# Optimization experiments

Measured on AMD Instinct MI355X. Metric: run time of the kernel, lower is better.

The kernel has to match this reference:

```python
import jax, jax.numpy as jnp
import numpy as np

MARGIN = 1.0
CURVATURE = 1.0
BOUNDARY_FACTOR = 2.0
MARGIN_THRESHOLD = 0.1
EPS = 1e-7


def setup_inputs() -> dict:
    key = jax.random.key(0)
    k1, k2 = jax.random.split(key)
    B, D = 4096, 128
    # scale so norms stay inside the unit Poincare ball (~0.57 on average)
    embeddings = jax.random.normal(k1, (B, D), dtype=jnp.float32) * 0.05
    labels = jax.random.randint(k2, (B,), 0, 64, dtype=jnp.int64)
    return {"embeddings": embeddings, "labels": labels}


def _poincare_distance_matrix(x, c):
    # d(x,y) = (1/sqrt(c)) * arccosh(1 + 2c||x-y||^2 / ((1-c||x||^2)(1-c||y||^2)))
    sq = jnp.sum(x * x, axis=-1)                       # [B]
    diff_sq = jnp.maximum(sq[:, None] + sq[None, :] - 2.0 * (x @ x.T), 0.0)
    denom = jnp.maximum((1.0 - c * sq[:, None]) * (1.0 - c * sq[None, :]), EPS)
    arg = 1.0 + 2.0 * c * diff_sq / denom
    return jnp.arccosh(jnp.maximum(arg, 1.0)) / jnp.sqrt(c)


def reference(embeddings, labels):
    B = embeddings.shape[0]
    distances = _poincare_distance_matrix(embeddings, CURVATURE)   # [B,B]

    same = labels[:, None] == labels[None, :]
    eye = jnp.eye(B, dtype=bool)
    positive_mask = same & ~eye
    negative_mask = ~same

    has_pos = jnp.any(positive_mask, axis=1)
    has_neg = jnp.any(negative_mask, axis=1)
    valid_anchor = has_pos & has_neg                               # [B]

    neg_inf = jnp.asarray(-jnp.inf, distances.dtype)
    hardest_pos = jnp.max(jnp.where(positive_mask, distances, neg_inf), axis=1)
    hardest_pos = jnp.where(has_pos, hardest_pos, 0.0)

    # adaptive margin (torch uses .item() -> detached from autograd)
    anchor_norm = jax.lax.stop_gradient(jnp.linalg.norm(embeddings, axis=-1))
    margin = jnp.maximum(MARGIN * (1.0 + BOUNDARY_FACTOR * anchor_norm),
                         MARGIN_THRESHOLD)                          # [B]

    pair_mask = valid_anchor[:, None] & negative_mask               # [B,B]
    raw = hardest_pos[:, None] - distances + margin[:, None]
    losses = jnp.maximum(raw, 0.0)

    total_triplets = jnp.sum(pair_mask)
    num_active = jnp.sum((raw > 0.0) & pair_mask)
    denom = jnp.maximum(total_triplets, 1).astype(losses.dtype)
    loss = jnp.sum(jnp.where(pair_mask, losses, 0.0)) / denom       # 'mean'

    active_ratio = num_active.astype(jnp.float32) / jnp.maximum(
        total_triplets.astype(jnp.float32), 1.0)
    pos_count = jnp.sum(positive_mask)
    mean_distance = jnp.where(
        pos_count > 0,
        jnp.sum(jnp.where(positive_mask, distances, 0.0))
        / jnp.maximum(pos_count, 1).astype(distances.dtype),
        0.0)

    return (loss, num_active, total_triplets, active_ratio, mean_distance)
```

## Files before the change

kernel.cpp:

```cpp
#include <hip/hip_runtime.h>
#include <hip/hip_bf16.h>
#include <math.h>

static constexpr int D        = 128;
static constexpr int NL       = 64;
static constexpr int NT       = 64;
static constexpr int NT2      = 128;
static constexpr int LIDX_CAP = 512;

typedef __attribute__((ext_vector_type(8))) short  bf16x8;
typedef __attribute__((ext_vector_type(4))) float  f32x4;

__device__ __forceinline__ float wave_reduce_sum(float v) {
  #pragma unroll
  for (int o = 32; o; o >>= 1) v += __shfl_xor(v, o, 64);
  return v;
}

__device__ __forceinline__ float fast_acosh(float x) {
  float s = __builtin_amdgcn_sqrtf(fmaf(x, x, -1.0f));
  return __logf(x + s);
}

__device__ __forceinline__ unsigned short f2b(float x) {
  unsigned int u = __float_as_uint(x);
  unsigned int lsb = (u >> 16) & 1u;
  u += 0x7fffu + lsb;
  return (unsigned short)(u >> 16);
}
__device__ __forceinline__ float b2f(unsigned short u) {
  return __uint_as_float(((unsigned int)u) << 16);
}

__global__ __launch_bounds__(256) void kA(
    const float* __restrict__ emb, const int* __restrict__ lab,
    unsigned short* __restrict__ bfe, float* __restrict__ sq,
    float* __restrict__ vv, float* __restrict__ hpm,
    int* __restrict__ LC, float* __restrict__ plsum, int B) {
  const int t = threadIdx.x;
  const int bid = blockIdx.x;

  if (bid >= NL) {
    int w = t >> 6, lane = t & 63;
    int i = (bid - NL) * 4 + w;
    float2 v = reinterpret_cast<const float2*>(emb + (size_t)i * D)[lane];
    ushort2 bv = { f2b(v.x), f2b(v.y) };
    *reinterpret_cast<ushort2*>(&bfe[(size_t)i * D + 2 * lane]) = bv;
    float s = wave_reduce_sum(v.x * v.x + v.y * v.y);
    if (lane == 0) {
      sq[i] = s;
      vv[i] = 1.41421356237f / fmaxf(1.0f - s, 1e-6f);
    }
    return;
  }

  __shared__ unsigned short Al[NT][D + 8];
  __shared__ unsigned short Bl[NT][D + 8];
  __shared__ float rs[NT], rv[NT];
  __shared__ float cs[NT], cv[NT];
  __shared__ int   ridx[NT], cidx[NT];
  __shared__ int   lidx[LIDX_CAP];
  __shared__ int   parr[256];
  __shared__ float red[8];

  const int l = bid;
  const int wid = t >> 6, lane = t & 63;
  const int lr = lane & 15, lg = lane >> 4;

  int mc = 0;
  for (int i = t; i < B; i += 256) mc += (lab[i] == l) ? 1 : 0;
  parr[t] = mc;
  __syncthreads();
  for (int off = 1; off < 256; off <<= 1) {
    int v = (t >= off) ? parr[t - off] : 0;
    __syncthreads();
    parr[t] += v;
    __syncthreads();
  }
  const int c = parr[255];
  {
    int myoff = parr[t] - mc;
    for (int i = t; i < B; i += 256) {
      if (lab[i] == l) {
        if (myoff < LIDX_CAP) lidx[myoff] = i;
        ++myoff;
      }
    }
  }
  if (t == 0) { LC[l] = c; if (c == 0) plsum[l] = 0.0f; }
  if (c == 0) return;
  __syncthreads();

  const int  cc_    = min(c, LIDX_CAP);
  const bool validc = (c >= 2) && (c < B);
  float lsum = 0.0f;

  for (int i0 = 0; i0 < cc_; i0 += NT) {
    int ci = min(NT, cc_ - i0);
    __syncthreads();
    #pragma unroll
    for (int p = 0; p < 4; ++p) {
      int idx = t + p * 256;
      int r = idx >> 4, c16 = idx & 15;
      const float* src = emb + (size_t)lidx[i0 + min(r, ci - 1)] * D + c16 * 8;
      float4 a = *reinterpret_cast<const float4*>(src);
      float4 b = *reinterpret_cast<const float4*>(src + 4);
      ushort4 ua = { f2b(a.x), f2b(a.y), f2b(a.z), f2b(a.w) };
      ushort4 ub = { f2b(b.x), f2b(b.y), f2b(b.z), f2b(b.w) };
      *reinterpret_cast<ushort4*>(&Al[r][c16 * 8]) = ua;
      *reinterpret_cast<ushort4*>(&Al[r][c16 * 8 + 4]) = ub;
    }
    __syncthreads();
    {
      int r = t >> 2, q = t & 3;
      float s = 0.0f;
      #pragma unroll
      for (int i = 0; i < 4; ++i) {
        bf16x8 v8 = *reinterpret_cast<const bf16x8*>(&Al[r][q * 32 + i * 8]);
        #pragma unroll
        for (int j = 0; j < 8; ++j) {
          float x = b2f((unsigned short)v8[j]);
          s = fmaf(x, x, s);
        }
      }
      s += __shfl_xor(s, 1, 64);
      s += __shfl_xor(s, 2, 64);
      if (q == 0) {
        rs[r] = s;
        rv[r] = 1.41421356237f / fmaxf(1.0f - s, 1e-6f);
        ridx[r] = lidx[i0 + min(r, ci - 1)];
      }
    }

    float rmax[4] = {0.0f, 0.0f, 0.0f, 0.0f};

    for (int j0 = 0; j0 < cc_; j0 += NT) {
      int cj = min(NT, cc_ - j0);
      __syncthreads();
      #pragma unroll
      for (int p = 0; p < 4; ++p) {
        int idx = t + p * 256;
        int r = idx >> 4, c16 = idx & 15;
        const float* src = emb + (size_t)lidx[j0 + min(r, cj - 1)] * D + c16 * 8;
        float4 a = *reinterpret_cast<const float4*>(src);
        float4 b = *reinterpret_cast<const float4*>(src + 4);
        ushort4 ua = { f2b(a.x), f2b(a.y), f2b(a.z), f2b(a.w) };
        ushort4 ub = { f2b(b.x), f2b(b.y), f2b(b.z), f2b(b.w) };
        *reinterpret_cast<ushort4*>(&Bl[r][c16 * 8]) = ua;
        *reinterpret_cast<ushort4*>(&Bl[r][c16 * 8 + 4]) = ub;
      }
      __syncthreads();
      {
        int r = t >> 2, q = t & 3;
        float s = 0.0f;
        #pragma unroll
        for (int i = 0; i < 4; ++i) {
          bf16x8 v8 = *reinterpret_cast<const bf16x8*>(&Bl[r][q * 32 + i * 8]);
          #pragma unroll
          for (int j = 0; j < 8; ++j) {
            float x = b2f((unsigned short)v8[j]);
            s = fmaf(x, x, s);
          }
        }
        s += __shfl_xor(s, 1, 64);
        s += __shfl_xor(s, 2, 64);
        if (q == 0) {
          cs[r] = s;
          cv[r] = 1.41421356237f / fmaxf(1.0f - s, 1e-6f);
          cidx[r] = lidx[j0 + min(r, cj - 1)];
        }
      }
      __syncthreads();

      f32x4 dacc[4];
      #pragma unroll
      for (int n = 0; n < 4; ++n) dacc[n] = (f32x4){0.f, 0.f, 0.f, 0.f};
      #pragma unroll
      for (int kk = 0; kk < 4; ++kk) {
        bf16x8 a = *reinterpret_cast<const bf16x8*>(&Al[wid * 16 + lr][kk * 32 + lg * 8]);
        bf16x8 b[4];
        #pragma unroll
        for (int n = 0; n < 4; ++n)
          b[n] = *reinterpret_cast<const bf16x8*>(&Bl[n * 16 + lr][kk * 32 + lg * 8]);
        #pragma unroll
        for (int n = 0; n < 4; ++n)
          dacc[n] = __builtin_amdgcn_mfma_f32_16x16x32_bf16(a, b[n], dacc[n], 0, 0, 0);
      }

      int r0 = wid * 16 + lg * 4;
      #pragma unroll
      for (int n = 0; n < 4; ++n) {
        int ccn = n * 16 + lr;
        float sc = cs[ccn], vcv = cv[ccn];
        int   gj = cidx[ccn];
        #pragma unroll
        for (int g = 0; g < 4; ++g) {
          int rloc = r0 + g;
          if (rloc < ci && ccn < cj && ridx[rloc] != gj) {
            float diff = fmaxf(fmaf(-2.0f, dacc[n][g], rs[rloc] + sc), 0.0f);
            float arg  = fmaf(diff * rv[rloc], vcv, 1.0f);
            float d    = fast_acosh(arg);
            lsum += d;
            rmax[g] = fmaxf(rmax[g], d);
          }
        }
      }
    }

    int r0 = wid * 16 + lg * 4;
    #pragma unroll
    for (int g = 0; g < 4; ++g) {
      float v = rmax[g];
      v = fmaxf(v, __shfl_xor(v, 1, 64));
      v = fmaxf(v, __shfl_xor(v, 2, 64));
      v = fmaxf(v, __shfl_xor(v, 4, 64));
      v = fmaxf(v, __shfl_xor(v, 8, 64));
      int rloc = r0 + g;
      if (lr == 0 && rloc < ci) {
        float mg = fmaxf(fmaf(2.0f, __builtin_amdgcn_sqrtf(rs[rloc]), 1.0f), 0.1f);
        hpm[ridx[rloc]] = validc ? (v + mg) : -1e30f;
      }
    }
  }

  lsum = wave_reduce_sum(lsum);
  if (lane == 0) red[wid] = lsum;
  __syncthreads();
  if (t == 0) plsum[l] = (red[0] + red[1]) + (red[2] + red[3]);
}

__global__ __launch_bounds__(512) void k3_neg(
    const unsigned short* __restrict__ bfe, const int* __restrict__ lab,
    const float* __restrict__ sq, const float* __restrict__ vv,
    const float* __restrict__ hpm,
    float* __restrict__ part, int B) {
  __shared__ unsigned short Al[NT2][D + 8];
  __shared__ unsigned short Bl[NT2][D + 8];
  __shared__ float rs[NT2], rv[NT2], rh[NT2];
  __shared__ float cs[NT2], cv[NT2], ch[NT2];
  __shared__ int   rl[NT2], cl[NT2];
  __shared__ float red[16];

  const int T2 = B / NT2;
  const int t = threadIdx.x;
  const int wid = t >> 6, lane = t & 63;
  const int wr = wid >> 2, wc = wid & 3;
  const int lr = lane & 15, lg = lane >> 4;
  const int bid = blockIdx.x;

  float disc = (float)((2 * T2 + 1) * (2 * T2 + 1) - 8 * bid);
  int bi = (int)(((float)(2 * T2 + 1) - __builtin_amdgcn_sqrtf(disc)) * 0.5f);
  bi = max(0, min(bi, T2 - 1));
  while (bi * T2 - bi * (bi - 1) / 2 > bid) --bi;
  while ((bi + 1) * T2 - (bi + 1) * bi / 2 <= bid) ++bi;
  int bj = bi + (bid - (bi * T2 - bi * (bi - 1) / 2));
  const float dsec = (bi == bj) ? 0.0f : 1.0f;

  const unsigned short* ab = bfe + (size_t)bi * NT2 * D;
  const unsigned short* bb = bfe + (size_t)bj * NT2 * D;
  #pragma unroll
  for (int p = 0; p < 4; ++p) {
    int idx = t + p * 512;
    int r = idx >> 4, c16 = idx & 15;
    bf16x8 va = reinterpret_cast<const bf16x8*>(ab + (size_t)r * D)[c16];
    bf16x8 vb = reinterpret_cast<const bf16x8*>(bb + (size_t)r * D)[c16];
    *reinterpret_cast<bf16x8*>(&Al[r][c16 * 8]) = va;
    *reinterpret_cast<bf16x8*>(&Bl[r][c16 * 8]) = vb;
  }
  if (t < NT2) {
    int g = bi * NT2 + t;
    rs[t] = sq[g]; rv[t] = vv[g]; rh[t] = hpm[g]; rl[t] = lab[g];
  } else if (t < 2 * NT2) {
    int r = t - NT2, g = bj * NT2 + r;
    cs[r] = sq[g]; cv[r] = vv[g]; ch[r] = hpm[g]; cl[r] = lab[g];
  }
  __syncthreads();

  f32x4 dacc[4][2];
  #pragma unroll
  for (int m = 0; m < 4; ++m)
    #pragma unroll
    for (int n = 0; n < 2; ++n) dacc[m][n] = (f32x4){0.f, 0.f, 0.f, 0.f};

  #pragma unroll
  for (int kk = 0; kk < 4; ++kk) {
    bf16x8 a[4], b[2];
    #pragma unroll
    for (int m = 0; m < 4; ++m)
      a[m] = *reinterpret_cast<const bf16x8*>(&Al[wr * 64 + m * 16 + lr][kk * 32 + lg * 8]);
    #pragma unroll
    for (int n = 0; n < 2; ++n)
      b[n] = *reinterpret_cast<const bf16x8*>(&Bl[wc * 32 + n * 16 + lr][kk * 32 + lg * 8]);
    #pragma unroll
    for (int m = 0; m < 4; ++m)
      #pragma unroll
      for (int n = 0; n < 2; ++n)
        dacc[m][n] = __builtin_amdgcn_mfma_f32_16x16x32_bf16(a[m], b[n], dacc[m][n], 0, 0, 0);
  }

  float nsum = 0.0f, nact = 0.0f;
  #pragma unroll
  for (int m = 0; m < 4; ++m) {
    int r0 = wr * 64 + m * 16 + lg * 4;
    f32x4 sr = *reinterpret_cast<const f32x4*>(&rs[r0]);
    f32x4 vr = *reinterpret_cast<const f32x4*>(&rv[r0]);
    f32x4 hr = *reinterpret_cast<const f32x4*>(&rh[r0]);
    int4  lm = *reinterpret_cast<const int4*>(&rl[r0]);
    int lmv[4] = { lm.x, lm.y, lm.z, lm.w };
    #pragma unroll
    for (int n = 0; n < 2; ++n) {
      int ccn = wc * 32 + n * 16 + lr;
      float sc = cs[ccn], vcv = cv[ccn], hc = ch[ccn];
      int   lc = cl[ccn];
      #pragma unroll
      for (int g = 0; g < 4; ++g) {
        float diff = fmaxf(fmaf(-2.0f, dacc[m][n][g], sr[g] + sc), 0.0f);
        float arg  = fmaf(diff * vr[g], vcv, 1.0f);
        float d    = fast_acosh(arg);
        float r1   = hr[g] - d;
        float r2   = hc    - d;
        float neg  = (lmv[g] != lc) ? 1.0f : 0.0f;
        nsum += neg * (fmaxf(r1, 0.0f) + dsec * fmaxf(r2, 0.0f));
        nact += neg * ((r1 > 0.0f ? 1.0f : 0.0f) + dsec * (r2 > 0.0f ? 1.0f : 0.0f));
      }
    }
  }

  nsum = wave_reduce_sum(nsum);
  nact = wave_reduce_sum(nact);
  if (lane == 0) { red[wid] = nsum; red[8 + wid] = nact; }
  __syncthreads();
  if (t == 0) {
    float S = 0.0f, A = 0.0f;
    #pragma unroll
    for (int w = 0; w < 8; ++w) { S += red[w]; A += red[8 + w]; }
    part[2 * bid]     = S;
    part[2 * bid + 1] = A;
  }
}

__global__ __launch_bounds__(256) void k4_final(
    const float* __restrict__ part, int G,
    const int* __restrict__ LC, const float* __restrict__ plsum,
    float* __restrict__ out, int B) {
  __shared__ float sl[256], sa[256];
  __shared__ float fin[3];
  int t = threadIdx.x;
  float s = 0.0f, a = 0.0f;
  for (int i = t; i < G; i += 256) {
    s += part[2 * i];
    a += part[2 * i + 1];
  }
  sl[t] = s; sa[t] = a;
  __syncthreads();
  for (int o = 128; o; o >>= 1) {
    if (t < o) { sl[t] += sl[t + o]; sa[t] += sa[t + o]; }
    __syncthreads();
  }
  if (t < 64) {
    int   c  = LC[t];
    float cf = (float)c;
    float pc = cf * (cf - 1.0f);
    float tr = ((c >= 2) && (c < B)) ? cf * (float)(B - c) : 0.0f;
    float ps = plsum[t];
    pc = wave_reduce_sum(pc);
    tr = wave_reduce_sum(tr);
    ps = wave_reduce_sum(ps);
    if (t == 0) { fin[0] = pc; fin[1] = tr; fin[2] = ps; }
  }
  __syncthreads();
  if (t == 0) {
    float PC = fin[0], TR = fin[1], PS = fin[2];
    float den = fmaxf(TR, 1.0f);
    out[0] = sl[0] / den;
    out[1] = sa[0];
    out[2] = TR;
    out[3] = sa[0] / den;
    out[4] = (PC > 0.0f) ? PS / fmaxf(PC, 1.0f) : 0.0f;
  }
}

extern "C" void kernel_launch(void* const* d_in, const int* in_sizes, int n_in,
                              void* d_out, int out_size, void* d_ws, size_t ws_size,
                              hipStream_t stream) {
  const float* emb = (const float*)d_in[0];
  const int*   lab = (const int*)d_in[1];
  int B = in_sizes[1];

  int T2 = B / NT2;
  int ntile = T2 * (T2 + 1) / 2;

  unsigned short* bfe = (unsigned short*)d_ws;
  float* sq    = (float*)(bfe + (size_t)B * D);
  float* vv    = sq + B;
  float* hpm   = vv + B;
  int*   LC    = (int*)(hpm + B);
  float* plsum = (float*)(LC + NL);
  float* part  = plsum + NL;

  kA<<<NL + B / 4, 256, 0, stream>>>(emb, lab, bfe, sq, vv, hpm, LC, plsum, B);
  k3_neg<<<ntile, 512, 0, stream>>>(bfe, lab, sq, vv, hpm, part, B);
  k4_final<<<1, 256, 0, stream>>>(part, ntile, LC, plsum, (float*)d_out, B);
}
```

Baseline: 44.19 us.

## Make pairwise tile kernel persistent with register-prefetched next tile

The negative-pair kernel now launches a fixed grid of 512 blocks that stride over the 528 upper-triangular tiles instead of one block per tile. While storing the current tile's bf16 rows and per-row scalars to shared memory, each block issues global loads for its next tile into registers, so load latency can overlap compute. The final reduction now sums only G partials. Since 528 is only slightly more than 512, most blocks process one tile and a few process two, which can lengthen the tail, and the prefetch registers raise register pressure.

```diff
diff --git a/kernel.cpp b/kernel.cpp
--- a/kernel.cpp
+++ b/kernel.cpp
@@ -233,7 +233,7 @@
     const unsigned short* __restrict__ bfe, const int* __restrict__ lab,
     const float* __restrict__ sq, const float* __restrict__ vv,
     const float* __restrict__ hpm,
-    float* __restrict__ part, int B) {
+    float* __restrict__ part, int B, int G) {
   __shared__ unsigned short Al[NT2][D + 8];
   __shared__ unsigned short Bl[NT2][D + 8];
   __shared__ float rs[NT2], rv[NT2], rh[NT2];
@@ -242,88 +242,127 @@
   __shared__ float red[16];
 
   const int T2 = B / NT2;
+  const int ntile = T2 * (T2 + 1) / 2;
   const int t = threadIdx.x;
   const int wid = t >> 6, lane = t & 63;
   const int wr = wid >> 2, wc = wid & 3;
   const int lr = lane & 15, lg = lane >> 4;
   const int bid = blockIdx.x;
 
-  float disc = (float)((2 * T2 + 1) * (2 * T2 + 1) - 8 * bid);
-  int bi = (int)(((float)(2 * T2 + 1) - __builtin_amdgcn_sqrtf(disc)) * 0.5f);
-  bi = max(0, min(bi, T2 - 1));
-  while (bi * T2 - bi * (bi - 1) / 2 > bid) --bi;
-  while ((bi + 1) * T2 - (bi + 1) * bi / 2 <= bid) ++bi;
-  int bj = bi + (bid - (bi * T2 - bi * (bi - 1) / 2));
-  const float dsec = (bi == bj) ? 0.0f : 1.0f;
-
-  const unsigned short* ab = bfe + (size_t)bi * NT2 * D;
-  const unsigned short* bb = bfe + (size_t)bj * NT2 * D;
-  #pragma unroll
-  for (int p = 0; p < 4; ++p) {
-    int idx = t + p * 512;
-    int r = idx >> 4, c16 = idx & 15;
-    bf16x8 va = reinterpret_cast<const bf16x8*>(ab + (size_t)r * D)[c16];
-    bf16x8 vb = reinterpret_cast<const bf16x8*>(bb + (size_t)r * D)[c16];
-    *reinterpret_cast<bf16x8*>(&Al[r][c16 * 8]) = va;
-    *reinterpret_cast<bf16x8*>(&Bl[r][c16 * 8]) = vb;
-  }
-  if (t < NT2) {
-    int g = bi * NT2 + t;
-    rs[t] = sq[g]; rv[t] = vv[g]; rh[t] = hpm[g]; rl[t] = lab[g];
-  } else if (t < 2 * NT2) {
-    int r = t - NT2, g = bj * NT2 + r;
-    cs[r] = sq[g]; cv[r] = vv[g]; ch[r] = hpm[g]; cl[r] = lab[g];
-  }
-  __syncthreads();
-
-  f32x4 dacc[4][2];
-  #pragma unroll
-  for (int m = 0; m < 4; ++m)
-    #pragma unroll
-    for (int n = 0; n < 2; ++n) dacc[m][n] = (f32x4){0.f, 0.f, 0.f, 0.f};
-
-  #pragma unroll
-  for (int kk = 0; kk < 4; ++kk) {
-    bf16x8 a[4], b[2];
+  bf16x8 pre[8];
+  float ps0 = 0, ps1 = 0, ps2 = 0;
+  int   ps3 = 0;
+  float nsum = 0.0f, nact = 0.0f;
+
+  auto decode = [&](int tile, int& bi, int& bj) {
+    float disc = (float)((2 * T2 + 1) * (2 * T2 + 1) - 8 * tile);
+    int b = (int)(((float)(2 * T2 + 1) - __builtin_amdgcn_sqrtf(disc)) * 0.5f);
+    b = max(0, min(b, T2 - 1));
+    while (b * T2 - b * (b - 1) / 2 > tile) --b;
+    while ((b + 1) * T2 - (b + 1) * b / 2 <= tile) ++b;
+    bi = b;
+    bj = b + (tile - (b * T2 - b * (b - 1) / 2));
+  };
+
+  auto load_tile = [&](int bi, int bj) {
+    const unsigned short* ab = bfe + (size_t)bi * NT2 * D;
+    const unsigned short* bb = bfe + (size_t)bj * NT2 * D;
+    #pragma unroll
+    for (int p = 0; p < 4; ++p) {
+      int idx = t + p * 512;
+      int r = idx >> 4, c16 = idx & 15;
+      pre[p]     = reinterpret_cast<const bf16x8*>(ab + (size_t)r * D)[c16];
+      pre[4 + p] = reinterpret_cast<const bf16x8*>(bb + (size_t)r * D)[c16];
+    }
+    if (t < NT2) {
+      int g = bi * NT2 + t;
+      ps0 = sq[g]; ps1 = vv[g]; ps2 = hpm[g]; ps3 = lab[g];
+    } else if (t < 2 * NT2) {
+      int g = bj * NT2 + (t - NT2);
+      ps0 = sq[g]; ps1 = vv[g]; ps2 = hpm[g]; ps3 = lab[g];
+    }
+  };
+
+  int tile = bid;
+  if (tile >= ntile) return;
+  int bi, bj;
+  decode(tile, bi, bj);
+  float next_dsec = (bi == bj) ? 0.0f : 1.0f;
+  load_tile(bi, bj);
+
+  while (tile < ntile) {
+    const float dsec = next_dsec;
+    __syncthreads();
+    #pragma unroll
+    for (int p = 0; p < 4; ++p) {
+      int idx = t + p * 512;
+      int r = idx >> 4, c16 = idx & 15;
+      *reinterpret_cast<bf16x8*>(&Al[r][c16 * 8]) = pre[p];
+      *reinterpret_cast<bf16x8*>(&Bl[r][c16 * 8]) = pre[4 + p];
+    }
+    if (t < NT2) {
+      rs[t] = ps0; rv[t] = ps1; rh[t] = ps2; rl[t] = ps3;
+    } else if (t < 2 * NT2) {
+      int r = t - NT2;
+      cs[r] = ps0; cv[r] = ps1; ch[r] = ps2; cl[r] = ps3;
+    }
+    int tile_next = tile + G;
+    if (tile_next < ntile) {
+      decode(tile_next, bi, bj);
+      next_dsec = (bi == bj) ? 0.0f : 1.0f;
+      load_tile(bi, bj);
+    }
+    __syncthreads();
+
+    f32x4 dacc[4][2];
     #pragma unroll
     for (int m = 0; m < 4; ++m)
-      a[m] = *reinterpret_cast<const bf16x8*>(&Al[wr * 64 + m * 16 + lr][kk * 32 + lg * 8]);
-    #pragma unroll
-    for (int n = 0; n < 2; ++n)
-      b[n] = *reinterpret_cast<const bf16x8*>(&Bl[wc * 32 + n * 16 + lr][kk * 32 + lg * 8]);
-    #pragma unroll
-    for (int m = 0; m < 4; ++m)
+      #pragma unroll
+      for (int n = 0; n < 2; ++n) dacc[m][n] = (f32x4){0.f, 0.f, 0.f, 0.f};
+
+    #pragma unroll
+    for (int kk = 0; kk < 4; ++kk) {
+      bf16x8 a[4], b[2];
+      #pragma unroll
+      for (int m = 0; m < 4; ++m)
+        a[m] = *reinterpret_cast<const bf16x8*>(&Al[wr * 64 + m * 16 + lr][kk * 32 + lg * 8]);
       #pragma unroll
       for (int n = 0; n < 2; ++n)
-        dacc[m][n] = __builtin_amdgcn_mfma_f32_16x16x32_bf16(a[m], b[n], dacc[m][n], 0, 0, 0);
-  }
-
-  float nsum = 0.0f, nact = 0.0f;
-  #pragma unroll
-  for (int m = 0; m < 4; ++m) {
-    int r0 = wr * 64 + m * 16 + lg * 4;
-    f32x4 sr = *reinterpret_cast<const f32x4*>(&rs[r0]);
-    f32x4 vr = *reinterpret_cast<const f32x4*>(&rv[r0]);
-    f32x4 hr = *reinterpret_cast<const f32x4*>(&rh[r0]);
-    int4  lm = *reinterpret_cast<const int4*>(&rl[r0]);
-    int lmv[4] = { lm.x, lm.y, lm.z, lm.w };
-    #pragma unroll
-    for (int n = 0; n < 2; ++n) {
-      int ccn = wc * 32 + n * 16 + lr;
-      float sc = cs[ccn], vcv = cv[ccn], hc = ch[ccn];
-      int   lc = cl[ccn];
-      #pragma unroll
-      for (int g = 0; g < 4; ++g) {
-        float diff = fmaxf(fmaf(-2.0f, dacc[m][n][g], sr[g] + sc), 0.0f);
-        float arg  = fmaf(diff * vr[g], vcv, 1.0f);
-        float d    = fast_acosh(arg);
-        float r1   = hr[g] - d;
-        float r2   = hc    - d;
-        float neg  = (lmv[g] != lc) ? 1.0f : 0.0f;
-        nsum += neg * (fmaxf(r1, 0.0f) + dsec * fmaxf(r2, 0.0f));
-        nact += neg * ((r1 > 0.0f ? 1.0f : 0.0f) + dsec * (r2 > 0.0f ? 1.0f : 0.0f));
-      }
-    }
+        b[n] = *reinterpret_cast<const bf16x8*>(&Bl[wc * 32 + n * 16 + lr][kk * 32 + lg * 8]);
+      #pragma unroll
+      for (int m = 0; m < 4; ++m)
+        #pragma unroll
+        for (int n = 0; n < 2; ++n)
+          dacc[m][n] = __builtin_amdgcn_mfma_f32_16x16x32_bf16(a[m], b[n], dacc[m][n], 0, 0, 0);
+    }
+
+    #pragma unroll
+    for (int m = 0; m < 4; ++m) {
+      int r0 = wr * 64 + m * 16 + lg * 4;
+      f32x4 sr = *reinterpret_cast<const f32x4*>(&rs[r0]);
+      f32x4 vr = *reinterpret_cast<const f32x4*>(&rv[r0]);
+      f32x4 hr = *reinterpret_cast<const f32x4*>(&rh[r0]);
+      int4  lm = *reinterpret_cast<const int4*>(&rl[r0]);
+      int lmv[4] = { lm.x, lm.y, lm.z, lm.w };
+      #pragma unroll
+      for (int n = 0; n < 2; ++n) {
+        int ccn = wc * 32 + n * 16 + lr;
+        float sc = cs[ccn], vcv = cv[ccn], hc = ch[ccn];
+        int   lc = cl[ccn];
+        #pragma unroll
+        for (int g = 0; g < 4; ++g) {
+          float diff = fmaxf(fmaf(-2.0f, dacc[m][n][g], sr[g] + sc), 0.0f);
+          float arg  = fmaf(diff * vr[g], vcv, 1.0f);
+          float d    = fast_acosh(arg);
+          float r1   = hr[g] - d;
+          float r2   = hc    - d;
+          float neg  = (lmv[g] != lc) ? 1.0f : 0.0f;
+          nsum += neg * (fmaxf(r1, 0.0f) + dsec * fmaxf(r2, 0.0f));
+          nact += neg * ((r1 > 0.0f ? 1.0f : 0.0f) + dsec * (r2 > 0.0f ? 1.0f : 0.0f));
+        }
+      }
+    }
+    tile = tile_next;
   }
 
   nsum = wave_reduce_sum(nsum);
@@ -389,6 +428,8 @@
 
   int T2 = B / NT2;
   int ntile = T2 * (T2 + 1) / 2;
+  int G = 512;
+  if (G > ntile) G = ntile;
 
   unsigned short* bfe = (unsigned short*)d_ws;
   float* sq    = (float*)(bfe + (size_t)B * D);
@@ -399,6 +440,6 @@
   float* part  = plsum + NL;
 
   kA<<<NL + B / 4, 256, 0, stream>>>(emb, lab, bfe, sq, vv, hpm, LC, plsum, B);
-  k3_neg<<<ntile, 512, 0, stream>>>(bfe, lab, sq, vv, hpm, part, B);
-  k4_final<<<1, 256, 0, stream>>>(part, ntile, LC, plsum, (float*)d_out, B);
-}
+  k3_neg<<<G, 512, 0, stream>>>(bfe, lab, sq, vv, hpm, part, B, G);
+  k4_final<<<1, 256, 0, stream>>>(part, G, LC, plsum, (float*)d_out, B);
+}
```

Result: slower. 46.73 us (+5.7%).
